# Kernel optimization log

Hardware: AMD Instinct MI355X
Metric: run time of the kernel (lower is better)

Reference implementation:

```python
import jax, jax.numpy as jnp
import numpy as np

N = 2048          # n_nodes
H = 8             # nheads
ALPHA = 0.2       # leaky-relu slope
NEG = -9e15       # mask value used by pyGAT
# (in_dim, per-head hidden, out_dim) for the six GAT blocks of GMHAAE(256, ...)
DIMS = [(256, 128, 128), (128, 256, 256), (256, 512, 384),
        (384, 512, 256), (256, 256, 128), (128, 128, 256)]


def setup_inputs() -> dict:
    key = jax.random.key(0)
    ks = jax.random.split(key, 64)
    inp = {}
    inp["x"] = jax.random.normal(ks[0], (N, 256), dtype=jnp.float32)
    a = (jax.random.uniform(ks[1], (N, N)) < 0.01).astype(jnp.float32)
    adj = jnp.clip(jnp.maximum(a, a.T) + jnp.eye(N, dtype=jnp.float32), 0.0, 1.0)
    inp["adj"] = adj
    ki = 2
    for i, (fin, hid, fout) in enumerate(DIMS, start=1):
        s1 = (2.0 / (fin + hid)) ** 0.5
        inp[f"p{i}_Wh"] = jax.random.normal(ks[ki], (H, fin, hid), dtype=jnp.float32) * s1; ki += 1
        inp[f"p{i}_ah"] = jax.random.normal(ks[ki], (H, 2 * hid), dtype=jnp.float32) * 0.1; ki += 1
        s2 = (2.0 / (H * hid + fout)) ** 0.5
        inp[f"p{i}_Wo"] = jax.random.normal(ks[ki], (H * hid, fout), dtype=jnp.float32) * s2; ki += 1
        inp[f"p{i}_ao"] = jax.random.normal(ks[ki], (2 * fout,), dtype=jnp.float32) * 0.1; ki += 1
    return inp


def _gat_block(x, adj, Wh, ah, Wo, ao):
    """pyGAT GAT block: H concat heads (elu) -> single out head -> elu. Eval mode (no dropout)."""
    n = x.shape[0]
    D = Wh.shape[2]
    h = jnp.einsum('nf,hfd->hnd', x, Wh)                       # [H,N,D]
    s1 = jnp.einsum('hnd,hd->hn', h, ah[:, :D])                # a^T [Wh_i]
    s2 = jnp.einsum('hnd,hd->hn', h, ah[:, D:])                # a^T [Wh_j]
    e = jax.nn.leaky_relu(s1[:, :, None] + s2[:, None, :], ALPHA)   # [H,N,N]
    att = jax.nn.softmax(jnp.where(adj[None] > 0, e, NEG), axis=-1)
    hcat = jax.nn.elu(jnp.einsum('hnm,hmd->hnd', att, h))      # concat=True -> elu per head
    hcat = hcat.transpose(1, 0, 2).reshape(n, -1)              # [N, H*D]
    # output attention head (concat=False)
    D2 = Wo.shape[1]
    ho = hcat @ Wo                                             # [N,D2]
    eo = jax.nn.leaky_relu((ho @ ao[:D2])[:, None] + (ho @ ao[D2:])[None, :], ALPHA)
    ato = jax.nn.softmax(jnp.where(adj > 0, eo, NEG), axis=-1)
    return jax.nn.elu(ato @ ho)                                # F.elu in GAT.forward


def reference(x, adj,
              p1_Wh, p1_ah, p1_Wo, p1_ao,
              p2_Wh, p2_ah, p2_Wo, p2_ao,
              p3_Wh, p3_ah, p3_Wo, p3_ao,
              p4_Wh, p4_ah, p4_Wo, p4_ao,
              p5_Wh, p5_ah, p5_Wo, p5_ao,
              p6_Wh, p6_ah, p6_Wo, p6_ao):
    layers = [(p1_Wh, p1_ah, p1_Wo, p1_ao), (p2_Wh, p2_ah, p2_Wo, p2_ao),
              (p3_Wh, p3_ah, p3_Wo, p3_ao), (p4_Wh, p4_ah, p4_Wo, p4_ao),
              (p5_Wh, p5_ah, p5_Wo, p5_ao), (p6_Wh, p6_ah, p6_Wo, p6_ao)]
    h = x
    for (Wh, ah, Wo, ao) in layers:   # fixed 6-layer encoder-decoder stack
        h = _gat_block(h, adj, Wh, ah, Wo, ao)
    return h
```

## Files before the change

### kernel.cpp

```cpp
#include <hip/hip_runtime.h>
#include <hip/hip_bf16.h>
#include <math.h>

#define NN 2048
#define NH 8
#define LRALPHA 0.2f

typedef short bf16x8 __attribute__((ext_vector_type(8)));
typedef float f32x4  __attribute__((ext_vector_type(4)));

static __device__ __forceinline__ float lrelu(float x){ return x > 0.f ? x : LRALPHA * x; }
static __device__ __forceinline__ float elu(float x){ return x > 0.f ? x : expm1f(x); }

static __device__ __forceinline__ unsigned short f2bf(float v){
    unsigned u = __float_as_uint(v);
    unsigned r = (u + 0x7fffu + ((u >> 16) & 1u)) >> 16;
    return (unsigned short)r;
}
static __device__ __forceinline__ float bf2f(unsigned short b){
    return __uint_as_float(((unsigned)b) << 16);
}
static __device__ __forceinline__ float blo(unsigned u){ return __uint_as_float(u << 16); }
static __device__ __forceinline__ float bhi(unsigned u){ return __uint_as_float(u & 0xffff0000u); }

static __device__ __forceinline__ void gload16(const void* g, void* l){
    __builtin_amdgcn_global_load_lds((const __attribute__((address_space(1))) void*)g,
                                     (__attribute__((address_space(3))) void*)l, 16, 0, 0);
}

__global__ void k_count(const float* __restrict__ adj, int* __restrict__ deg) {
    int gw   = (blockIdx.x * blockDim.x + threadIdx.x) >> 6;
    int lane = threadIdx.x & 63;
    if (gw >= NN) return;
    const float* row = adj + (size_t)gw * NN;
    int cnt = 0;
    for (int j = lane; j < NN; j += 64) cnt += (row[j] > 0.f) ? 1 : 0;
    #pragma unroll
    for (int off = 32; off; off >>= 1) cnt += __shfl_down(cnt, off);
    if (lane == 0) deg[gw] = cnt;
}

__global__ void k_scan(const int* __restrict__ deg, int* __restrict__ rp) {
    __shared__ int a[NN], b[NN];
    int t = threadIdx.x;
    for (int i = t; i < NN; i += 1024) a[i] = deg[i];
    __syncthreads();
    int* src = a; int* dst = b;
    for (int off = 1; off < NN; off <<= 1) {
        for (int i = t; i < NN; i += 1024)
            dst[i] = src[i] + (i >= off ? src[i - off] : 0);
        __syncthreads();
        int* tmp = src; src = dst; dst = tmp;
    }
    for (int i = t; i < NN; i += 1024) rp[i + 1] = src[i];
    if (t == 0) rp[0] = 0;
}

__global__ void k_fill(const float* __restrict__ adj, const int* __restrict__ rp,
                       int* __restrict__ ci) {
    int gw   = (blockIdx.x * blockDim.x + threadIdx.x) >> 6;
    int lane = threadIdx.x & 63;
    if (gw >= NN) return;
    const float* row = adj + (size_t)gw * NN;
    int base = rp[gw];
    for (int j0 = 0; j0 < NN; j0 += 64) {
        bool v = row[j0 + lane] > 0.f;
        unsigned long long m = __ballot(v);
        int pos = __popcll(m & ((1ULL << lane) - 1ULL));
        if (v) ci[base + pos] = j0 + lane;
        base += __popcll(m);
    }
}

__global__ void k_split(const float* __restrict__ src, unsigned short* __restrict__ hi,
                        unsigned short* __restrict__ lo, int n4) {
    int i = blockIdx.x * 256 + threadIdx.x;
    if (i >= n4) return;
    float4 v = ((const float4*)src)[i];
    ushort4 h, l;
    h.x = f2bf(v.x); l.x = f2bf(v.x - bf2f(h.x));
    h.y = f2bf(v.y); l.y = f2bf(v.y - bf2f(h.y));
    h.z = f2bf(v.z); l.z = f2bf(v.z - bf2f(h.z));
    h.w = f2bf(v.w); l.w = f2bf(v.w - bf2f(h.w));
    ((ushort4*)hi)[i] = h;
    ((ushort4*)lo)[i] = l;
}

struct TSDesc {
    const float* B[12];
    unsigned short* bh[12];
    unsigned short* bl[12];
    int K[12], Nc[12], hs[12];
    int start[13];
};

__global__ __launch_bounds__(256) void k_tsplit_all(TSDesc d) {
    __shared__ float t[64][65];
    int b = blockIdx.x;
    int s = 0;
    while (b >= d.start[s + 1]) s++;
    int lb = b - d.start[s];
    int K = d.K[s], Nc = d.Nc[s], hs = d.hs[s];
    int tilesX = K >> 6;
    int kb = (lb % tilesX) * 64, cb = (lb / tilesX) * 64;
    const float* B = d.B[s];
    unsigned short* bth = d.bh[s];
    unsigned short* btl = d.bl[s];

    int tid = threadIdx.x;
    #pragma unroll
    for (int i = 0; i < 16; i++) {
        int idx = i * 256 + tid;
        int kk = idx >> 6, cc = idx & 63;
        int c = cb + cc, k = kb + kk;
        float v;
        if (hs < 0) v = B[(size_t)k * Nc + c];
        else {
            int hid = 1 << hs; int head = c >> hs; int dd = c & (hid - 1);
            v = B[((size_t)head * K + k) * hid + dd];
        }
        t[kk][cc] = v;
    }
    __syncthreads();
    #pragma unroll
    for (int i = 0; i < 16; i++) {
        int idx = i * 256 + tid;
        int cc = idx >> 6, kk = idx & 63;
        float v = t[kk][cc];
        unsigned short h = f2bf(v);
        size_t o = (size_t)(cb + cc) * K + kb + kk;
        bth[o] = h;
        btl[o] = f2bf(v - bf2f(h));
    }
}

template<int OUT, int NT>
__global__ __launch_bounds__(256) void k_mfma(
    const unsigned short* __restrict__ Ah, const unsigned short* __restrict__ Al,
    const unsigned short* __restrict__ Bh, const unsigned short* __restrict__ Bl,
    float* __restrict__ Cf, unsigned short* __restrict__ Cb, int Nc, int K, int Kc,
    const float* __restrict__ avec, float* __restrict__ sg1, float* __restrict__ sg2,
    int hs, int aoff, int nx, int nz, int zcol)
{
    constexpr int ALB = 4096;
    constexpr int BHB = (NT == 3) ? 8192 : 4096;
    constexpr int BLB = BHB + 2048;
    __shared__ unsigned short lds[(NT == 3) ? 12288 : 8192];
    int tid = threadIdx.x, lane = tid & 63, w = tid >> 6;

    int g = blockIdx.x;
    int xcd = g & 7, q = g >> 3;
    int x, y, z;
    if (zcol) {
        int zper = nz >> 3;
        z = xcd + 8 * (q % zper);
        int r = q / zper;
        int nxy = nx * 16;
        int r2 = r + xcd * (nxy >> 3); if (r2 >= nxy) r2 -= nxy;
        x = r2 % nx; y = r2 / nx;
    } else {
        y = xcd + 8 * (q & 1);
        x = q >> 1; z = 0;
    }
    int m0 = y * 128, n0 = x * 64;
    int kbeg = z * Kc;

    int ra0 = tid >> 2;       int ga0 = ((tid & 3) - (ra0 >> 1)) & 3;
    int ra1 = 64 + (tid >> 2); int ga1 = ((tid & 3) - (ra1 >> 1)) & 3;
    int rb  = tid >> 2;       int gb  = ((tid & 3) - (rb >> 1)) & 3;
    const unsigned short* pAh0 = Ah + (size_t)(m0 + ra0) * K + kbeg + ga0 * 8;
    const unsigned short* pAh1 = Ah + (size_t)(m0 + ra1) * K + kbeg + ga1 * 8;
    const unsigned short* pAl0 = (NT == 3) ? Al + (size_t)(m0 + ra0) * K + kbeg + ga0 * 8 : nullptr;
    const unsigned short* pAl1 = (NT == 3) ? Al + (size_t)(m0 + ra1) * K + kbeg + ga1 * 8 : nullptr;
    const unsigned short* pBh  = Bh + (size_t)(n0 + rb) * K + kbeg + gb * 8;
    const unsigned short* pBl  = Bl + (size_t)(n0 + rb) * K + kbeg + gb * 8;
    unsigned short* dA0 = &lds[w * 512];
    unsigned short* dA1 = &lds[2048 + w * 512];
    unsigned short* dB  = &lds[BHB + w * 512];

    int wr = w >> 1, wc = w & 1;
    int offA[4], offB[2];
    #pragma unroll
    for (int m = 0; m < 4; m++) {
        int row = wr * 64 + m * 16 + (lane & 15); int gg = lane >> 4;
        offA[m] = (row * 4 + ((gg + (row >> 1)) & 3)) * 8;
    }
    #pragma unroll
    for (int n = 0; n < 2; n++) {
        int row = wc * 32 + n * 16 + (lane & 15); int gg = lane >> 4;
        offB[n] = (row * 4 + ((gg + (row >> 1)) & 3)) * 8;
    }

    f32x4 acc[4][2];
    #pragma unroll
    for (int m = 0; m < 4; m++)
        #pragma unroll
        for (int n = 0; n < 2; n++) acc[m][n] = (f32x4){0.f, 0.f, 0.f, 0.f};

    int nk = Kc >> 5;
    for (int ks = 0; ks < nk; ks++) {
        gload16(pAh0, dA0);
        gload16(pAh1, dA1);
        if (NT == 3) { gload16(pAl0, dA0 + ALB); gload16(pAl1, dA1 + ALB); }
        gload16(pBh, dB);
        gload16(pBl, dB + 2048);
        pAh0 += 32; pAh1 += 32;
        if (NT == 3) { pAl0 += 32; pAl1 += 32; }
        pBh += 32; pBl += 32;
        __syncthreads();
        bf16x8 ah[4], al[4], bh[2], bl[2];
        #pragma unroll
        for (int m = 0; m < 4; m++) {
            ah[m] = *(const bf16x8*)&lds[offA[m]];
            if (NT == 3) al[m] = *(const bf16x8*)&lds[ALB + offA[m]];
        }
        #pragma unroll
        for (int n = 0; n < 2; n++) {
            bh[n] = *(const bf16x8*)&lds[BHB + offB[n]];
            bl[n] = *(const bf16x8*)&lds[BLB + offB[n]];
        }
        #pragma unroll
        for (int m = 0; m < 4; m++)
            #pragma unroll
            for (int n = 0; n < 2; n++) {
                acc[m][n] = __builtin_amdgcn_mfma_f32_16x16x32_bf16(ah[m], bh[n], acc[m][n], 0, 0, 0);
                if (NT == 3)
                    acc[m][n] = __builtin_amdgcn_mfma_f32_16x16x32_bf16(al[m], bh[n], acc[m][n], 0, 0, 0);
                acc[m][n] = __builtin_amdgcn_mfma_f32_16x16x32_bf16(ah[m], bl[n], acc[m][n], 0, 0, 0);
            }
        __syncthreads();
    }

    size_t pbase = (size_t)z * NN * Nc;
    #pragma unroll
    for (int m = 0; m < 4; m++)
        #pragma unroll
        for (int n = 0; n < 2; n++) {
            int row = m0 + wr * 64 + m * 16 + (lane >> 4) * 4;
            int col = n0 + wc * 32 + n * 16 + (lane & 15);
            #pragma unroll
            for (int r = 0; r < 4; r++) {
                float v = acc[m][n][r];
                if (OUT == 0) Cb[(size_t)(row + r) * Nc + col] = f2bf(v);
                else          Cf[pbase + (size_t)(row + r) * Nc + col] = v;
            }
        }

    if (OUT == 0) {
        int head = (hs >= 0) ? (n0 >> hs) : 0;
        const float* ab = avec + head * 2 * aoff;
        float av1[2], av2[2];
        int colbase = n0 + wc * 32 + (lane & 15);
        #pragma unroll
        for (int n = 0; n < 2; n++) {
            int c = colbase + n * 16;
            int dd = (hs >= 0) ? (c & (aoff - 1)) : c;
            av1[n] = ab[dd];
            av2[n] = ab[dd + aoff];
        }
        #pragma unroll
        for (int m = 0; m < 4; m++)
            #pragma unroll
            for (int r = 0; r < 4; r++) {
                float p1 = 0.f, p2 = 0.f;
                #pragma unroll
                for (int n = 0; n < 2; n++) {
                    float v = acc[m][n][r];
                    p1 += v * av1[n];
                    p2 += v * av2[n];
                }
                #pragma unroll
                for (int o = 1; o < 16; o <<= 1) {
                    p1 += __shfl_xor(p1, o);
                    p2 += __shfl_xor(p2, o);
                }
                if ((lane & 15) == 0) {
                    int row = m0 + wr * 64 + m * 16 + (lane >> 4) * 4 + r;
                    atomicAdd(&sg1[head * NN + row], p1);
                    atomicAdd(&sg2[head * NN + row], p2);
                }
            }
    }
}

__global__ __launch_bounds__(64) void k_red(
    const float* __restrict__ part, float* __restrict__ ho,
    const float* __restrict__ ao, float* __restrict__ t1, float* __restrict__ t2,
    int fout, int sko)
{
    int row = blockIdx.x;
    int lane = threadIdx.x;
    int C4 = fout >> 2;
    const float4* p4 = (const float4*)part;
    size_t stride4 = (size_t)NN * C4;
    float d1 = 0.f, d2 = 0.f;
    for (int c = lane; c < C4; c += 64) {
        size_t o = (size_t)row * C4 + c;
        float4 s = p4[o];
        for (int zz = 1; zz < sko; zz++) {
            float4 v = p4[o + (size_t)zz * stride4];
            s.x += v.x; s.y += v.y; s.z += v.z; s.w += v.w;
        }
        ((float4*)ho)[o] = s;
        int cc = c * 4;
        d1 += s.x * ao[cc]        + s.y * ao[cc + 1]
            + s.z * ao[cc + 2]    + s.w * ao[cc + 3];
        d2 += s.x * ao[fout + cc]     + s.y * ao[fout + cc + 1]
            + s.z * ao[fout + cc + 2] + s.w * ao[fout + cc + 3];
    }
    #pragma unroll
    for (int o = 32; o; o >>= 1) { d1 += __shfl_xor(d1, o); d2 += __shfl_xor(d2, o); }
    if (lane == 0) { t1[row] = d1; t2[row] = d2; }
}

__global__ __launch_bounds__(64) void k_aggb(
    const unsigned short* __restrict__ hh, const float* __restrict__ s1,
    const float* __restrict__ s2, const int* __restrict__ rp, const int* __restrict__ ci,
    unsigned short* __restrict__ outH, int hid, int HD, int c8sh)
{
    __shared__ float    wls[64];
    __shared__ unsigned cls[64];

    int blk  = blockIdx.x;
    int head = blk & (NH - 1);
    int i    = blk >> 3;
    int lane = threadIdx.x;
    int base = rp[i], deg = rp[i + 1] - base;
    float s1i = s1[head * NN + i];
    const float* s2h = s2 + head * NN;

    int C8  = 1 << c8sh;
    int G   = 64 >> c8sh;
    int col = lane & (C8 - 1);
    int grp = lane >> c8sh;

    const uint4* h4 = (const uint4*)hh;
    unsigned hoff8 = (unsigned)(head * hid) >> 3;
    unsigned ld8   = (unsigned)HD >> 3;

    float m_run = -1e30f, s_run = 0.f;
    float a0=0,a1=0,a2=0,a3=0,a4=0,a5=0,a6=0,a7=0;

    for (int k0 = 0; k0 < deg; k0 += 64) {
        int n = min(64, deg - k0);
        float e = -1e30f;
        unsigned coff = 0;
        if (lane < n) {
            int j = ci[base + k0 + lane];
            e = lrelu(s1i + s2h[j]);
            coff = (unsigned)j * ld8 + hoff8;
        }
        float bm = e;
        #pragma unroll
        for (int o = 32; o; o >>= 1) bm = fmaxf(bm, __shfl_xor(bm, o));
        float m2 = fmaxf(m_run, bm);
        float wv = (lane < n) ? expf(e - m2) : 0.f;
        float bs = wv;
        #pragma unroll
        for (int o = 32; o; o >>= 1) bs += __shfl_xor(bs, o);
        float scale = expf(m_run - m2);
        s_run = s_run * scale + bs;
        a0*=scale; a1*=scale; a2*=scale; a3*=scale;
        a4*=scale; a5*=scale; a6*=scale; a7*=scale;
        m_run = m2;
        wls[lane] = wv;
        cls[lane] = coff;

        float q0=0,q1=0,q2=0,q3=0,q4=0,q5=0,q6=0,q7=0;
        int k = grp;
        for (; k + G < n; k += 2 * G) {
            float w0 = wls[k], w1 = wls[k + G];
            uint4 u0 = h4[cls[k]     + col];
            uint4 u1 = h4[cls[k + G] + col];
            a0 += w0 * blo(u0.x); a1 += w0 * bhi(u0.x);
            a2 += w0 * blo(u0.y); a3 += w0 * bhi(u0.y);
            a4 += w0 * blo(u0.z); a5 += w0 * bhi(u0.z);
            a6 += w0 * blo(u0.w); a7 += w0 * bhi(u0.w);
            q0 += w1 * blo(u1.x); q1 += w1 * bhi(u1.x);
            q2 += w1 * blo(u1.y); q3 += w1 * bhi(u1.y);
            q4 += w1 * blo(u1.z); q5 += w1 * bhi(u1.z);
            q6 += w1 * blo(u1.w); q7 += w1 * bhi(u1.w);
        }
        if (k < n) {
            float w0 = wls[k];
            uint4 u0 = h4[cls[k] + col];
            a0 += w0 * blo(u0.x); a1 += w0 * bhi(u0.x);
            a2 += w0 * blo(u0.y); a3 += w0 * bhi(u0.y);
            a4 += w0 * blo(u0.z); a5 += w0 * bhi(u0.z);
            a6 += w0 * blo(u0.w); a7 += w0 * bhi(u0.w);
        }
        a0+=q0; a1+=q1; a2+=q2; a3+=q3; a4+=q4; a5+=q5; a6+=q6; a7+=q7;
    }

    #pragma unroll
    for (int o = 64; o > 1; o >>= 1) {
        if (o > C8) {
            int m = o >> 1;
            a0 += __shfl_xor(a0, m); a1 += __shfl_xor(a1, m);
            a2 += __shfl_xor(a2, m); a3 += __shfl_xor(a3, m);
            a4 += __shfl_xor(a4, m); a5 += __shfl_xor(a5, m);
            a6 += __shfl_xor(a6, m); a7 += __shfl_xor(a7, m);
        }
    }

    if (grp == 0) {
        float inv = 1.f / s_run;
        float v[8] = {a0*inv,a1*inv,a2*inv,a3*inv,a4*inv,a5*inv,a6*inv,a7*inv};
        #pragma unroll
        for (int e2 = 0; e2 < 8; e2++) v[e2] = elu(v[e2]);
        unsigned short hh_[8];
        #pragma unroll
        for (int e2 = 0; e2 < 8; e2++) hh_[e2] = f2bf(v[e2]);
        size_t ob = ((size_t)i * HD + head * hid) >> 3;
        uint4 ph;
        ph.x = (unsigned)hh_[0] | ((unsigned)hh_[1] << 16);
        ph.y = (unsigned)hh_[2] | ((unsigned)hh_[3] << 16);
        ph.z = (unsigned)hh_[4] | ((unsigned)hh_[5] << 16);
        ph.w = (unsigned)hh_[6] | ((unsigned)hh_[7] << 16);
        ((uint4*)outH)[ob + col] = ph;
    }
}

__global__ __launch_bounds__(64) void k_aggs(
    const float* __restrict__ hsrc, const float* __restrict__ t1, const float* __restrict__ t2,
    const int* __restrict__ rp, const int* __restrict__ ci,
    float* __restrict__ outF, unsigned short* __restrict__ outH,
    int fout, int SCtot)
{
    __shared__ float    wls[64];
    __shared__ unsigned cls[64];

    int blk = blockIdx.x;
    int i   = blk / SCtot;
    int sc  = blk - i * SCtot;
    int lane = threadIdx.x;
    int base = rp[i], deg = rp[i + 1] - base;
    float s1i = t1[i];

    int C4tot = fout >> 2;
    int soff  = sc * 64;
    int C4s   = min(64, C4tot - soff);
    int c4sh  = 31 - __clz(C4s);
    int col = lane & (C4s - 1);
    int grp = lane >> c4sh;
    int G   = 64 >> c4sh;

    const float4* h4 = (const float4*)hsrc;
    unsigned ld4 = (unsigned)fout >> 2;

    float m_run = -1e30f, s_run = 0.f;
    float4 acc = make_float4(0.f, 0.f, 0.f, 0.f);

    for (int k0 = 0; k0 < deg; k0 += 64) {
        int n = min(64, deg - k0);
        float e = -1e30f;
        unsigned coff = 0;
        if (lane < n) {
            int j = ci[base + k0 + lane];
            e = lrelu(s1i + t2[j]);
            coff = (unsigned)j * ld4 + soff;
        }
        float bm = e;
        #pragma unroll
        for (int o = 32; o; o >>= 1) bm = fmaxf(bm, __shfl_xor(bm, o));
        float m2 = fmaxf(m_run, bm);
        float wv = (lane < n) ? expf(e - m2) : 0.f;
        float bs = wv;
        #pragma unroll
        for (int o = 32; o; o >>= 1) bs += __shfl_xor(bs, o);
        float scale = expf(m_run - m2);
        s_run = s_run * scale + bs;
        acc.x *= scale; acc.y *= scale; acc.z *= scale; acc.w *= scale;
        m_run = m2;
        wls[lane] = wv;
        cls[lane] = coff;

        float4 q = make_float4(0,0,0,0);
        int k = grp;
        for (; k + G < n; k += 2 * G) {
            float w0 = wls[k], w1 = wls[k + G];
            float4 h0 = h4[cls[k]     + col];
            float4 h1 = h4[cls[k + G] + col];
            acc.x += w0 * h0.x; acc.y += w0 * h0.y; acc.z += w0 * h0.z; acc.w += w0 * h0.w;
            q.x   += w1 * h1.x; q.y   += w1 * h1.y; q.z   += w1 * h1.z; q.w   += w1 * h1.w;
        }
        if (k < n) {
            float w0 = wls[k];
            float4 h0 = h4[cls[k] + col];
            acc.x += w0 * h0.x; acc.y += w0 * h0.y; acc.z += w0 * h0.z; acc.w += w0 * h0.w;
        }
        acc.x += q.x; acc.y += q.y; acc.z += q.z; acc.w += q.w;
    }

    #pragma unroll
    for (int o = 64; o > 1; o >>= 1) {
        if (o > C4s) {
            int m = o >> 1;
            acc.x += __shfl_xor(acc.x, m); acc.y += __shfl_xor(acc.y, m);
            acc.z += __shfl_xor(acc.z, m); acc.w += __shfl_xor(acc.w, m);
        }
    }

    if (grp == 0) {
        float inv = 1.f / s_run;
        float4 val;
        val.x = elu(acc.x * inv); val.y = elu(acc.y * inv);
        val.z = elu(acc.z * inv); val.w = elu(acc.w * inv);
        size_t o4 = (size_t)i * ld4 + soff + col;
        if (outF) ((float4*)outF)[o4] = val;
        ushort4 h;
        h.x = f2bf(val.x); h.y = f2bf(val.y);
        h.z = f2bf(val.z); h.w = f2bf(val.w);
        ((ushort4*)outH)[o4] = h;
    }
}

extern "C" void kernel_launch(void* const* d_in, const int* in_sizes, int n_in,
                              void* d_out, int out_size, void* d_ws, size_t ws_size,
                              hipStream_t stream)
{
    const float* x   = (const float*)d_in[0];
    const float* adj = (const float*)d_in[1];
    struct L { int fin, hid, fout; };
    const L dims[6] = {{256,128,128},{128,256,256},{256,512,384},
                       {384,512,256},{256,256,128},{128,128,256}};
    const int SKwo[6] = {16, 8, 8, 8, 16, 8};
    const int SB = 2 * NH * NN;

    char* ws = (char*)d_ws;
    size_t off = 0;
    auto alloc = [&](size_t bytes) -> void* {
        void* p = ws + off;
        off = (off + bytes + 255) & ~(size_t)255;
        return p;
    };
    int*   rp   = (int*)alloc((NN + 1) * sizeof(int));
    int*   deg  = (int*)alloc(NN * sizeof(int));
    int*   ci   = (int*)alloc((size_t)(1 << 20) * sizeof(int));
    unsigned short* hh  = (unsigned short*)alloc((size_t)NN * 4096 * 2);
    unsigned short* ghi = (unsigned short*)alloc((size_t)NN * 4096 * 2);
    unsigned short* xhi = (unsigned short*)alloc((size_t)NN * 512 * 2);
    unsigned short* xlo = (unsigned short*)alloc((size_t)NN * 512 * 2);
    float* sball  = (float*)alloc((size_t)6 * SB * sizeof(float));
    float* hopart = (float*)alloc((size_t)NN * 3072 * sizeof(float));
    float* ho     = (float*)alloc((size_t)NN * 384 * sizeof(float));
    float* t12    = (float*)alloc((size_t)2 * NN * sizeof(float));

    unsigned short* whh[6]; unsigned short* whl[6];
    unsigned short* woh[6]; unsigned short* wol[6];
    TSDesc td;
    int nblk = 0;
    for (int l = 0; l < 6; l++) {
        int fin = dims[l].fin, hid = dims[l].hid, fout = dims[l].fout;
        int HD = NH * hid;
        size_t szWh = (size_t)fin * HD, szWo = (size_t)HD * fout;
        whh[l] = (unsigned short*)alloc(szWh * 2);
        whl[l] = (unsigned short*)alloc(szWh * 2);
        woh[l] = (unsigned short*)alloc(szWo * 2);
        wol[l] = (unsigned short*)alloc(szWo * 2);
        int hs = (hid == 128) ? 7 : (hid == 256) ? 8 : 9;
        td.B[2*l] = (const float*)d_in[2 + l * 4 + 0];
        td.bh[2*l] = whh[l]; td.bl[2*l] = whl[l];
        td.K[2*l] = fin; td.Nc[2*l] = HD; td.hs[2*l] = hs;
        td.start[2*l] = nblk; nblk += (fin / 64) * (HD / 64);
        td.B[2*l+1] = (const float*)d_in[2 + l * 4 + 2];
        td.bh[2*l+1] = woh[l]; td.bl[2*l+1] = wol[l];
        td.K[2*l+1] = HD; td.Nc[2*l+1] = fout; td.hs[2*l+1] = -1;
        td.start[2*l+1] = nblk; nblk += (HD / 64) * (fout / 64);
    }
    td.start[12] = nblk;

    hipMemsetAsync(sball, 0, (size_t)6 * SB * sizeof(float), stream);
    k_count<<<NN / 4, 256, 0, stream>>>(adj, deg);
    k_scan <<<1, 1024, 0, stream>>>(deg, rp);
    k_fill <<<NN / 4, 256, 0, stream>>>(adj, rp, ci);
    k_split<<<(NN * 256 / 4 + 255) / 256, 256, 0, stream>>>(x, xhi, xlo, NN * 256 / 4);
    k_tsplit_all<<<nblk, 256, 0, stream>>>(td);

    for (int l = 0; l < 6; l++) {
        int fin = dims[l].fin, hid = dims[l].hid, fout = dims[l].fout;
        int HD = NH * hid;
        int hs = (hid == 128) ? 7 : (hid == 256) ? 8 : 9;
        int c8sh = hs - 3;
        const float* ah = (const float*)d_in[2 + l * 4 + 1];
        const float* ao = (const float*)d_in[2 + l * 4 + 3];

        float* s1 = sball + (size_t)l * SB;
        float* s2 = s1 + NH * NN;
        float* t1 = t12;
        float* t2 = t12 + NN;

        int nx1 = HD / 64;
        if (l == 0)
            k_mfma<0,3><<<nx1 * 16, 256, 0, stream>>>(xhi, xlo, whh[l], whl[l], nullptr, hh, HD,
                                                      fin, fin, ah, s1, s2, hs, hid, nx1, 1, 0);
        else
            k_mfma<0,2><<<nx1 * 16, 256, 0, stream>>>(xhi, nullptr, whh[l], whl[l], nullptr, hh, HD,
                                                      fin, fin, ah, s1, s2, hs, hid, nx1, 1, 0);

        k_aggb<<<NN * NH, 64, 0, stream>>>(hh, s1, s2, rp, ci, ghi, hid, HD, c8sh);

        int sko = SKwo[l];
        int nx2 = fout / 64;
        k_mfma<1,2><<<nx2 * 16 * sko, 256, 0, stream>>>(ghi, nullptr, woh[l], wol[l], hopart,
                                                        nullptr, fout, HD, HD / sko,
                                                        nullptr, nullptr, nullptr, -1, fout,
                                                        nx2, sko, 1);

        k_red<<<NN, 64, 0, stream>>>(hopart, ho, ao, t1, t2, fout, sko);

        float* outF = (l == 5) ? (float*)d_out : nullptr;
        int SCtot = (fout / 4 + 63) / 64;
        k_aggs<<<NN * SCtot, 64, 0, stream>>>(ho, t1, t2, rp, ci, outF, xhi, fout, SCtot);
    }
}
```

Baseline: 449.6 us.

## Double GEMM K-tile to 64 and widen per-lane columns in aggregation kernels

The MFMA GEMM now stages a 64-wide K slice per iteration, using a new 8-group XOR swizzle. This halves the number of barrier pairs per K loop at the cost of twice the LDS footprint. The two sparse-attention aggregation kernels now have each lane handle 16 bf16 or 8 fp32 columns instead of 8 or 4. That gives each lane more independent loads and more groups over neighbours, but raises register pressure and adds shuffle-reduction steps.

```diff
diff --git a/kernel.cpp b/kernel.cpp
--- a/kernel.cpp
+++ b/kernel.cpp
@@ -27,6 +27,12 @@
     __builtin_amdgcn_global_load_lds((const __attribute__((address_space(1))) void*)g,
                                      (__attribute__((address_space(3))) void*)l, 16, 0, 0);
 }
+
+#define ACC8(A, base, wv, u) \
+    A[base+0] += wv * blo(u.x); A[base+1] += wv * bhi(u.x); \
+    A[base+2] += wv * blo(u.y); A[base+3] += wv * bhi(u.y); \
+    A[base+4] += wv * blo(u.z); A[base+5] += wv * bhi(u.z); \
+    A[base+6] += wv * blo(u.w); A[base+7] += wv * bhi(u.w);
 
 __global__ void k_count(const float* __restrict__ adj, int* __restrict__ deg) {
     int gw   = (blockIdx.x * blockDim.x + threadIdx.x) >> 6;
@@ -142,10 +148,10 @@
     const float* __restrict__ avec, float* __restrict__ sg1, float* __restrict__ sg2,
     int hs, int aoff, int nx, int nz, int zcol)
 {
-    constexpr int ALB = 4096;
-    constexpr int BHB = (NT == 3) ? 8192 : 4096;
-    constexpr int BLB = BHB + 2048;
-    __shared__ unsigned short lds[(NT == 3) ? 12288 : 8192];
+    constexpr int ALB = 8192;
+    constexpr int BHB = (NT == 3) ? 16384 : 8192;
+    constexpr int BLB = BHB + 4096;
+    __shared__ unsigned short lds[(NT == 3) ? 24576 : 16384];
     int tid = threadIdx.x, lane = tid & 63, w = tid >> 6;
 
     int g = blockIdx.x;
@@ -165,30 +171,44 @@
     int m0 = y * 128, n0 = x * 64;
     int kbeg = z * Kc;
 
-    int ra0 = tid >> 2;       int ga0 = ((tid & 3) - (ra0 >> 1)) & 3;
-    int ra1 = 64 + (tid >> 2); int ga1 = ((tid & 3) - (ra1 >> 1)) & 3;
-    int rb  = tid >> 2;       int gb  = ((tid & 3) - (rb >> 1)) & 3;
-    const unsigned short* pAh0 = Ah + (size_t)(m0 + ra0) * K + kbeg + ga0 * 8;
-    const unsigned short* pAh1 = Ah + (size_t)(m0 + ra1) * K + kbeg + ga1 * 8;
-    const unsigned short* pAl0 = (NT == 3) ? Al + (size_t)(m0 + ra0) * K + kbeg + ga0 * 8 : nullptr;
-    const unsigned short* pAl1 = (NT == 3) ? Al + (size_t)(m0 + ra1) * K + kbeg + ga1 * 8 : nullptr;
-    const unsigned short* pBh  = Bh + (size_t)(n0 + rb) * K + kbeg + gb * 8;
-    const unsigned short* pBl  = Bl + (size_t)(n0 + rb) * K + kbeg + gb * 8;
-    unsigned short* dA0 = &lds[w * 512];
-    unsigned short* dA1 = &lds[2048 + w * 512];
-    unsigned short* dB  = &lds[BHB + w * 512];
+    const unsigned short* pA[4];
+    const unsigned short* pAl_[4];
+    const unsigned short* pB[2];
+    const unsigned short* pBl_[2];
+    #pragma unroll
+    for (int c = 0; c < 4; c++) {
+        int s = c * 256 + tid;
+        int row = s >> 3; int gl = ((s & 7) - row) & 7;
+        pA[c] = Ah + (size_t)(m0 + row) * K + kbeg + gl * 8;
+        if (NT == 3) pAl_[c] = Al + (size_t)(m0 + row) * K + kbeg + gl * 8;
+    }
+    #pragma unroll
+    for (int c = 0; c < 2; c++) {
+        int s = c * 256 + tid;
+        int row = s >> 3; int gl = ((s & 7) - row) & 7;
+        pB[c]   = Bh + (size_t)(n0 + row) * K + kbeg + gl * 8;
+        pBl_[c] = Bl + (size_t)(n0 + row) * K + kbeg + gl * 8;
+    }
 
     int wr = w >> 1, wc = w & 1;
-    int offA[4], offB[2];
+    int offA[4][2], offB[2][2];
     #pragma unroll
     for (int m = 0; m < 4; m++) {
-        int row = wr * 64 + m * 16 + (lane & 15); int gg = lane >> 4;
-        offA[m] = (row * 4 + ((gg + (row >> 1)) & 3)) * 8;
+        int row = wr * 64 + m * 16 + (lane & 15);
+        #pragma unroll
+        for (int kk = 0; kk < 2; kk++) {
+            int gl = (lane >> 4) + 4 * kk;
+            offA[m][kk] = row * 64 + (((gl + row) & 7) * 8);
+        }
     }
     #pragma unroll
     for (int n = 0; n < 2; n++) {
-        int row = wc * 32 + n * 16 + (lane & 15); int gg = lane >> 4;
-        offB[n] = (row * 4 + ((gg + (row >> 1)) & 3)) * 8;
+        int row = wc * 32 + n * 16 + (lane & 15);
+        #pragma unroll
+        for (int kk = 0; kk < 2; kk++) {
+            int gl = (lane >> 4) + 4 * kk;
+            offB[n][kk] = row * 64 + (((gl + row) & 7) * 8);
+        }
     }
 
     f32x4 acc[4][2];
@@ -197,37 +217,42 @@
         #pragma unroll
         for (int n = 0; n < 2; n++) acc[m][n] = (f32x4){0.f, 0.f, 0.f, 0.f};
 
-    int nk = Kc >> 5;
+    int nk = Kc >> 6;
     for (int ks = 0; ks < nk; ks++) {
-        gload16(pAh0, dA0);
-        gload16(pAh1, dA1);
-        if (NT == 3) { gload16(pAl0, dA0 + ALB); gload16(pAl1, dA1 + ALB); }
-        gload16(pBh, dB);
-        gload16(pBl, dB + 2048);
-        pAh0 += 32; pAh1 += 32;
-        if (NT == 3) { pAl0 += 32; pAl1 += 32; }
-        pBh += 32; pBl += 32;
+        #pragma unroll
+        for (int c = 0; c < 4; c++) { gload16(pA[c], &lds[c * 2048 + w * 512]); pA[c] += 64; }
+        if (NT == 3) {
+            #pragma unroll
+            for (int c = 0; c < 4; c++) { gload16(pAl_[c], &lds[ALB + c * 2048 + w * 512]); pAl_[c] += 64; }
+        }
+        #pragma unroll
+        for (int c = 0; c < 2; c++) { gload16(pB[c], &lds[BHB + c * 2048 + w * 512]); pB[c] += 64; }
+        #pragma unroll
+        for (int c = 0; c < 2; c++) { gload16(pBl_[c], &lds[BLB + c * 2048 + w * 512]); pBl_[c] += 64; }
         __syncthreads();
-        bf16x8 ah[4], al[4], bh[2], bl[2];
-        #pragma unroll
-        for (int m = 0; m < 4; m++) {
-            ah[m] = *(const bf16x8*)&lds[offA[m]];
-            if (NT == 3) al[m] = *(const bf16x8*)&lds[ALB + offA[m]];
-        }
-        #pragma unroll
-        for (int n = 0; n < 2; n++) {
-            bh[n] = *(const bf16x8*)&lds[BHB + offB[n]];
-            bl[n] = *(const bf16x8*)&lds[BLB + offB[n]];
-        }
-        #pragma unroll
-        for (int m = 0; m < 4; m++)
+        #pragma unroll
+        for (int kk = 0; kk < 2; kk++) {
+            bf16x8 ah[4], al[4], bh[2], bl[2];
+            #pragma unroll
+            for (int m = 0; m < 4; m++) {
+                ah[m] = *(const bf16x8*)&lds[offA[m][kk]];
+                if (NT == 3) al[m] = *(const bf16x8*)&lds[ALB + offA[m][kk]];
+            }
             #pragma unroll
             for (int n = 0; n < 2; n++) {
-                acc[m][n] = __builtin_amdgcn_mfma_f32_16x16x32_bf16(ah[m], bh[n], acc[m][n], 0, 0, 0);
-                if (NT == 3)
-                    acc[m][n] = __builtin_amdgcn_mfma_f32_16x16x32_bf16(al[m], bh[n], acc[m][n], 0, 0, 0);
-                acc[m][n] = __builtin_amdgcn_mfma_f32_16x16x32_bf16(ah[m], bl[n], acc[m][n], 0, 0, 0);
+                bh[n] = *(const bf16x8*)&lds[BHB + offB[n][kk]];
+                bl[n] = *(const bf16x8*)&lds[BLB + offB[n][kk]];
             }
+            #pragma unroll
+            for (int m = 0; m < 4; m++)
+                #pragma unroll
+                for (int n = 0; n < 2; n++) {
+                    acc[m][n] = __builtin_amdgcn_mfma_f32_16x16x32_bf16(ah[m], bh[n], acc[m][n], 0, 0, 0);
+                    if (NT == 3)
+                        acc[m][n] = __builtin_amdgcn_mfma_f32_16x16x32_bf16(al[m], bh[n], acc[m][n], 0, 0, 0);
+                    acc[m][n] = __builtin_amdgcn_mfma_f32_16x16x32_bf16(ah[m], bl[n], acc[m][n], 0, 0, 0);
+                }
+        }
         __syncthreads();
     }
 
@@ -316,7 +341,7 @@
 __global__ __launch_bounds__(64) void k_aggb(
     const unsigned short* __restrict__ hh, const float* __restrict__ s1,
     const float* __restrict__ s2, const int* __restrict__ rp, const int* __restrict__ ci,
-    unsigned short* __restrict__ outH, int hid, int HD, int c8sh)
+    unsigned short* __restrict__ outH, int hid, int HD, int c16sh)
 {
     __shared__ float    wls[64];
     __shared__ unsigned cls[64];
@@ -329,17 +354,19 @@
     float s1i = s1[head * NN + i];
     const float* s2h = s2 + head * NN;
 
-    int C8  = 1 << c8sh;
-    int G   = 64 >> c8sh;
-    int col = lane & (C8 - 1);
-    int grp = lane >> c8sh;
+    int C16 = 1 << c16sh;
+    int G   = 64 >> c16sh;
+    int col = lane & (C16 - 1);
+    int grp = lane >> c16sh;
 
     const uint4* h4 = (const uint4*)hh;
     unsigned hoff8 = (unsigned)(head * hid) >> 3;
     unsigned ld8   = (unsigned)HD >> 3;
 
     float m_run = -1e30f, s_run = 0.f;
-    float a0=0,a1=0,a2=0,a3=0,a4=0,a5=0,a6=0,a7=0;
+    float aA[16];
+    #pragma unroll
+    for (int e = 0; e < 16; e++) aA[e] = 0.f;
 
     for (int k0 = 0; k0 < deg; k0 += 64) {
         int n = min(64, deg - k0);
@@ -360,64 +387,60 @@
         for (int o = 32; o; o >>= 1) bs += __shfl_xor(bs, o);
         float scale = expf(m_run - m2);
         s_run = s_run * scale + bs;
-        a0*=scale; a1*=scale; a2*=scale; a3*=scale;
-        a4*=scale; a5*=scale; a6*=scale; a7*=scale;
+        #pragma unroll
+        for (int e2 = 0; e2 < 16; e2++) aA[e2] *= scale;
         m_run = m2;
         wls[lane] = wv;
         cls[lane] = coff;
 
-        float q0=0,q1=0,q2=0,q3=0,q4=0,q5=0,q6=0,q7=0;
+        float q[16];
+        #pragma unroll
+        for (int e2 = 0; e2 < 16; e2++) q[e2] = 0.f;
         int k = grp;
         for (; k + G < n; k += 2 * G) {
             float w0 = wls[k], w1 = wls[k + G];
-            uint4 u0 = h4[cls[k]     + col];
-            uint4 u1 = h4[cls[k + G] + col];
-            a0 += w0 * blo(u0.x); a1 += w0 * bhi(u0.x);
-            a2 += w0 * blo(u0.y); a3 += w0 * bhi(u0.y);
-            a4 += w0 * blo(u0.z); a5 += w0 * bhi(u0.z);
-            a6 += w0 * blo(u0.w); a7 += w0 * bhi(u0.w);
-            q0 += w1 * blo(u1.x); q1 += w1 * bhi(u1.x);
-            q2 += w1 * blo(u1.y); q3 += w1 * bhi(u1.y);
-            q4 += w1 * blo(u1.z); q5 += w1 * bhi(u1.z);
-            q6 += w1 * blo(u1.w); q7 += w1 * bhi(u1.w);
+            const uint4* r0 = h4 + cls[k]     + 2 * col;
+            const uint4* r1 = h4 + cls[k + G] + 2 * col;
+            uint4 u0 = r0[0], u1 = r0[1];
+            uint4 v0 = r1[0], v1 = r1[1];
+            ACC8(aA, 0, w0, u0); ACC8(aA, 8, w0, u1);
+            ACC8(q,  0, w1, v0); ACC8(q,  8, w1, v1);
         }
         if (k < n) {
             float w0 = wls[k];
-            uint4 u0 = h4[cls[k] + col];
-            a0 += w0 * blo(u0.x); a1 += w0 * bhi(u0.x);
-            a2 += w0 * blo(u0.y); a3 += w0 * bhi(u0.y);
-            a4 += w0 * blo(u0.z); a5 += w0 * bhi(u0.z);
-            a6 += w0 * blo(u0.w); a7 += w0 * bhi(u0.w);
-        }
-        a0+=q0; a1+=q1; a2+=q2; a3+=q3; a4+=q4; a5+=q5; a6+=q6; a7+=q7;
-    }
-
-    #pragma unroll
-    for (int o = 64; o > 1; o >>= 1) {
-        if (o > C8) {
-            int m = o >> 1;
-            a0 += __shfl_xor(a0, m); a1 += __shfl_xor(a1, m);
-            a2 += __shfl_xor(a2, m); a3 += __shfl_xor(a3, m);
-            a4 += __shfl_xor(a4, m); a5 += __shfl_xor(a5, m);
-            a6 += __shfl_xor(a6, m); a7 += __shfl_xor(a7, m);
+            const uint4* r0 = h4 + cls[k] + 2 * col;
+            uint4 u0 = r0[0], u1 = r0[1];
+            ACC8(aA, 0, w0, u0); ACC8(aA, 8, w0, u1);
+        }
+        #pragma unroll
+        for (int e2 = 0; e2 < 16; e2++) aA[e2] += q[e2];
+    }
+
+    #pragma unroll
+    for (int m = 32; m >= 1; m >>= 1) {
+        if (m >= C16) {
+            #pragma unroll
+            for (int e2 = 0; e2 < 16; e2++) aA[e2] += __shfl_xor(aA[e2], m);
         }
     }
 
     if (grp == 0) {
         float inv = 1.f / s_run;
-        float v[8] = {a0*inv,a1*inv,a2*inv,a3*inv,a4*inv,a5*inv,a6*inv,a7*inv};
-        #pragma unroll
-        for (int e2 = 0; e2 < 8; e2++) v[e2] = elu(v[e2]);
-        unsigned short hh_[8];
-        #pragma unroll
-        for (int e2 = 0; e2 < 8; e2++) hh_[e2] = f2bf(v[e2]);
-        size_t ob = ((size_t)i * HD + head * hid) >> 3;
-        uint4 ph;
-        ph.x = (unsigned)hh_[0] | ((unsigned)hh_[1] << 16);
-        ph.y = (unsigned)hh_[2] | ((unsigned)hh_[3] << 16);
-        ph.z = (unsigned)hh_[4] | ((unsigned)hh_[5] << 16);
-        ph.w = (unsigned)hh_[6] | ((unsigned)hh_[7] << 16);
-        ((uint4*)outH)[ob + col] = ph;
+        unsigned short hh_[16];
+        #pragma unroll
+        for (int e2 = 0; e2 < 16; e2++) hh_[e2] = f2bf(elu(aA[e2] * inv));
+        size_t ob = (((size_t)i * HD + head * hid) >> 3) + 2 * col;
+        uint4 p0, p1;
+        p0.x = (unsigned)hh_[0]  | ((unsigned)hh_[1]  << 16);
+        p0.y = (unsigned)hh_[2]  | ((unsigned)hh_[3]  << 16);
+        p0.z = (unsigned)hh_[4]  | ((unsigned)hh_[5]  << 16);
+        p0.w = (unsigned)hh_[6]  | ((unsigned)hh_[7]  << 16);
+        p1.x = (unsigned)hh_[8]  | ((unsigned)hh_[9]  << 16);
+        p1.y = (unsigned)hh_[10] | ((unsigned)hh_[11] << 16);
+        p1.z = (unsigned)hh_[12] | ((unsigned)hh_[13] << 16);
+        p1.w = (unsigned)hh_[14] | ((unsigned)hh_[15] << 16);
+        ((uint4*)outH)[ob]     = p0;
+        ((uint4*)outH)[ob + 1] = p1;
     }
 }
 
@@ -440,16 +463,19 @@
     int C4tot = fout >> 2;
     int soff  = sc * 64;
     int C4s   = min(64, C4tot - soff);
-    int c4sh  = 31 - __clz(C4s);
-    int col = lane & (C4s - 1);
-    int grp = lane >> c4sh;
-    int G   = 64 >> c4sh;
+    int C8s   = C4s >> 1;
+    int c8sh  = 31 - __clz(C8s);
+    int col = lane & (C8s - 1);
+    int grp = lane >> c8sh;
+    int G   = 64 >> c8sh;
 
     const float4* h4 = (const float4*)hsrc;
     unsigned ld4 = (unsigned)fout >> 2;
 
     float m_run = -1e30f, s_run = 0.f;
-    float4 acc = make_float4(0.f, 0.f, 0.f, 0.f);
+    float aA[8];
+    #pragma unroll
+    for (int e = 0; e < 8; e++) aA[e] = 0.f;
 
     for (int k0 = 0; k0 < deg; k0 += 64) {
         int n = min(64, deg - k0);
@@ -470,48 +496,61 @@
         for (int o = 32; o; o >>= 1) bs += __shfl_xor(bs, o);
         float scale = expf(m_run - m2);
         s_run = s_run * scale + bs;
-        acc.x *= scale; acc.y *= scale; acc.z *= scale; acc.w *= scale;
+        #pragma unroll
+        for (int e2 = 0; e2 < 8; e2++) aA[e2] *= scale;
         m_run = m2;
         wls[lane] = wv;
         cls[lane] = coff;
 
-        float4 q = make_float4(0,0,0,0);
+        float q[8];
+        #pragma unroll
+        for (int e2 = 0; e2 < 8; e2++) q[e2] = 0.f;
         int k = grp;
         for (; k + G < n; k += 2 * G) {
             float w0 = wls[k], w1 = wls[k + G];
-            float4 h0 = h4[cls[k]     + col];
-            float4 h1 = h4[cls[k + G] + col];
-            acc.x += w0 * h0.x; acc.y += w0 * h0.y; acc.z += w0 * h0.z; acc.w += w0 * h0.w;
-            q.x   += w1 * h1.x; q.y   += w1 * h1.y; q.z   += w1 * h1.z; q.w   += w1 * h1.w;
+            const float4* r0 = h4 + cls[k]     + 2 * col;
+            const float4* r1 = h4 + cls[k + G] + 2 * col;
+            float4 h0 = r0[0], h1 = r0[1];
+            float4 g0 = r1[0], g1 = r1[1];
+            aA[0] += w0 * h0.x; aA[1] += w0 * h0.y; aA[2] += w0 * h0.z; aA[3] += w0 * h0.w;
+            aA[4] += w0 * h1.x; aA[5] += w0 * h1.y; aA[6] += w0 * h1.z; aA[7] += w0 * h1.w;
+            q[0]  += w1 * g0.x; q[1]  += w1 * g0.y; q[2]  += w1 * g0.z; q[3]  += w1 * g0.w;
+            q[4]  += w1 * g1.x; q[5]  += w1 * g1.y; q[6]  += w1 * g1.z; q[7]  += w1 * g1.w;
         }
         if (k < n) {
             float w0 = wls[k];
-            float4 h0 = h4[cls[k] + col];
-            acc.x += w0 * h0.x; acc.y += w0 * h0.y; acc.z += w0 * h0.z; acc.w += w0 * h0.w;
-        }
-        acc.x += q.x; acc.y += q.y; acc.z += q.z; acc.w += q.w;
-    }
-
-    #pragma unroll
-    for (int o = 64; o > 1; o >>= 1) {
-        if (o > C4s) {
-            int m = o >> 1;
-            acc.x += __shfl_xor(acc.x, m); acc.y += __shfl_xor(acc.y, m);
-            acc.z += __shfl_xor(acc.z, m); acc.w += __shfl_xor(acc.w, m);
+            const float4* r0 = h4 + cls[k] + 2 * col;
+            float4 h0 = r0[0], h1 = r0[1];
+            aA[0] += w0 * h0.x; aA[1] += w0 * h0.y; aA[2] += w0 * h0.z; aA[3] += w0 * h0.w;
+            aA[4] += w0 * h1.x; aA[5] += w0 * h1.y; aA[6] += w0 * h1.z; aA[7] += w0 * h1.w;
+        }
+        #pragma unroll
+        for (int e2 = 0; e2 < 8; e2++) aA[e2] += q[e2];
+    }
+
+    #pragma unroll
+    for (int m = 32; m >= 1; m >>= 1) {
+        if (m >= C8s) {
+            #pragma unroll
+            for (int e2 = 0; e2 < 8; e2++) aA[e2] += __shfl_xor(aA[e2], m);
         }
     }
 
     if (grp == 0) {
         float inv = 1.f / s_run;
-        float4 val;
-        val.x = elu(acc.x * inv); val.y = elu(acc.y * inv);
-        val.z = elu(acc.z * inv); val.w = elu(acc.w * inv);
-        size_t o4 = (size_t)i * ld4 + soff + col;
-        if (outF) ((float4*)outF)[o4] = val;
-        ushort4 h;
-        h.x = f2bf(val.x); h.y = f2bf(val.y);
-        h.z = f2bf(val.z); h.w = f2bf(val.w);
-        ((ushort4*)outH)[o4] = h;
+        float v[8];
+        #pragma unroll
+        for (int e2 = 0; e2 < 8; e2++) v[e2] = elu(aA[e2] * inv);
+        size_t o4 = (size_t)i * ld4 + soff + 2 * col;
+        if (outF) {
+            ((float4*)outF)[o4]     = make_float4(v[0], v[1], v[2], v[3]);
+            ((float4*)outF)[o4 + 1] = make_float4(v[4], v[5], v[6], v[7]);
+        }
+        ushort4 h0, h1;
+        h0.x = f2bf(v[0]); h0.y = f2bf(v[1]); h0.z = f2bf(v[2]); h0.w = f2bf(v[3]);
+        h1.x = f2bf(v[4]); h1.y = f2bf(v[5]); h1.z = f2bf(v[6]); h1.w = f2bf(v[7]);
+        ((ushort4*)outH)[o4]     = h0;
+        ((ushort4*)outH)[o4 + 1] = h1;
     }
 }
 
@@ -581,7 +620,6 @@
         int fin = dims[l].fin, hid = dims[l].hid, fout = dims[l].fout;
         int HD = NH * hid;
         int hs = (hid == 128) ? 7 : (hid == 256) ? 8 : 9;
-        int c8sh = hs - 3;
         const float* ah = (const float*)d_in[2 + l * 4 + 1];
         const float* ao = (const float*)d_in[2 + l * 4 + 3];
 
@@ -598,7 +636,7 @@
             k_mfma<0,2><<<nx1 * 16, 256, 0, stream>>>(xhi, nullptr, whh[l], whl[l], nullptr, hh, HD,
                                                       fin, fin, ah, s1, s2, hs, hid, nx1, 1, 0);
 
-        k_aggb<<<NN * NH, 64, 0, stream>>>(hh, s1, s2, rp, ci, ghi, hid, HD, c8sh);
+        k_aggb<<<NN * NH, 64, 0, stream>>>(hh, s1, s2, rp, ci, ghi, hid, HD, hs - 4);
 
         int sko = SKwo[l];
         int nx2 = fout / 64;
```

Measured after the change: 467.5 us. +4.0%, slower.

## Process multiple heads per wave and four rows per block in head aggregation

Applied to the files above, without the earlier changes.

The sparse attention aggregation kernel now assigns HP heads to each wave, chosen from the hidden size so every lane owns a full 8-column chunk, and packs four node rows per 256-thread block. Neighbor indices are loaded once and shared across the heads a wave handles. Each lane now issues several independent gathers per step through a deeper templated unroll, which raises memory-level parallelism. In exchange, register pressure grows because every lane keeps 16 accumulators per head. Lanes in the softmax statistics loop also repeat the shuffle reductions once per head.

```diff
diff --git a/kernel.cpp b/kernel.cpp
--- a/kernel.cpp
+++ b/kernel.cpp
@@ -27,6 +27,12 @@
     __builtin_amdgcn_global_load_lds((const __attribute__((address_space(1))) void*)g,
                                      (__attribute__((address_space(3))) void*)l, 16, 0, 0);
 }
+
+#define ACC8(A, wv, u) \
+    A[0] += wv * blo(u.x); A[1] += wv * bhi(u.x); \
+    A[2] += wv * blo(u.y); A[3] += wv * bhi(u.y); \
+    A[4] += wv * blo(u.z); A[5] += wv * bhi(u.z); \
+    A[6] += wv * blo(u.w); A[7] += wv * bhi(u.w);
 
 __global__ void k_count(const float* __restrict__ adj, int* __restrict__ deg) {
     int gw   = (blockIdx.x * blockDim.x + threadIdx.x) >> 6;
@@ -313,111 +319,126 @@
     if (lane == 0) { t1[row] = d1; t2[row] = d2; }
 }
 
-__global__ __launch_bounds__(64) void k_aggb(
+template<int HP>
+__global__ __launch_bounds__(256) void k_aggb(
     const unsigned short* __restrict__ hh, const float* __restrict__ s1,
     const float* __restrict__ s2, const int* __restrict__ rp, const int* __restrict__ ci,
-    unsigned short* __restrict__ outH, int hid, int HD, int c8sh)
+    unsigned short* __restrict__ outH, int hid, int HD)
 {
-    __shared__ float    wls[64];
-    __shared__ unsigned cls[64];
-
-    int blk  = blockIdx.x;
-    int head = blk & (NH - 1);
-    int i    = blk >> 3;
-    int lane = threadIdx.x;
+    constexpr int NHG = NH / HP;
+    constexpr int D   = (HP == 1) ? 8 : (HP == 2) ? 4 : 2;
+    constexpr int C8  = 64 / HP;
+    constexpr int G   = HP;
+
+    __shared__ float    wls[4][HP][64];
+    __shared__ unsigned cls[4][64];
+
+    int tid = threadIdx.x, wid = tid >> 6, lane = tid & 63;
+    int hg = blockIdx.x & (NHG - 1);
+    int i  = (blockIdx.x / NHG) * 4 + wid;
+    int h0 = hg * HP;
+
     int base = rp[i], deg = rp[i + 1] - base;
-    float s1i = s1[head * NN + i];
-    const float* s2h = s2 + head * NN;
-
-    int C8  = 1 << c8sh;
-    int G   = 64 >> c8sh;
-    int col = lane & (C8 - 1);
-    int grp = lane >> c8sh;
+    float s1i[HP];
+    #pragma unroll
+    for (int p = 0; p < HP; p++) s1i[p] = s1[(h0 + p) * NN + i];
+
+    int col = lane & (C8 - 1), grp = lane >> (6 - (HP == 1 ? 0 : HP == 2 ? 1 : 2));
+    grp = lane / C8;
 
     const uint4* h4 = (const uint4*)hh;
-    unsigned hoff8 = (unsigned)(head * hid) >> 3;
-    unsigned ld8   = (unsigned)HD >> 3;
-
-    float m_run = -1e30f, s_run = 0.f;
-    float a0=0,a1=0,a2=0,a3=0,a4=0,a5=0,a6=0,a7=0;
+    unsigned ld8 = (unsigned)HD >> 3;
+    unsigned hoff8[HP];
+    #pragma unroll
+    for (int p = 0; p < HP; p++) hoff8[p] = ((unsigned)(h0 + p) * hid) >> 3;
+
+    float m_run[HP], s_run[HP], acc[HP][8], q[HP][8];
+    #pragma unroll
+    for (int p = 0; p < HP; p++) {
+        m_run[p] = -1e30f; s_run[p] = 0.f;
+        #pragma unroll
+        for (int e = 0; e < 8; e++) { acc[p][e] = 0.f; q[p][e] = 0.f; }
+    }
 
     for (int k0 = 0; k0 < deg; k0 += 64) {
         int n = min(64, deg - k0);
-        float e = -1e30f;
-        unsigned coff = 0;
-        if (lane < n) {
-            int j = ci[base + k0 + lane];
-            e = lrelu(s1i + s2h[j]);
-            coff = (unsigned)j * ld8 + hoff8;
-        }
-        float bm = e;
-        #pragma unroll
-        for (int o = 32; o; o >>= 1) bm = fmaxf(bm, __shfl_xor(bm, o));
-        float m2 = fmaxf(m_run, bm);
-        float wv = (lane < n) ? expf(e - m2) : 0.f;
-        float bs = wv;
-        #pragma unroll
-        for (int o = 32; o; o >>= 1) bs += __shfl_xor(bs, o);
-        float scale = expf(m_run - m2);
-        s_run = s_run * scale + bs;
-        a0*=scale; a1*=scale; a2*=scale; a3*=scale;
-        a4*=scale; a5*=scale; a6*=scale; a7*=scale;
-        m_run = m2;
-        wls[lane] = wv;
-        cls[lane] = coff;
-
-        float q0=0,q1=0,q2=0,q3=0,q4=0,q5=0,q6=0,q7=0;
+        bool act = lane < n;
+        int j = 0;
+        if (act) { j = ci[base + k0 + lane]; cls[wid][lane] = (unsigned)j * ld8; }
+        #pragma unroll
+        for (int p = 0; p < HP; p++) {
+            float e = act ? lrelu(s1i[p] + s2[(h0 + p) * NN + j]) : -1e30f;
+            float bm = e;
+            #pragma unroll
+            for (int o = 32; o; o >>= 1) bm = fmaxf(bm, __shfl_xor(bm, o));
+            float m2 = fmaxf(m_run[p], bm);
+            float wv = act ? expf(e - m2) : 0.f;
+            float bs = wv;
+            #pragma unroll
+            for (int o = 32; o; o >>= 1) bs += __shfl_xor(bs, o);
+            float scale = expf(m_run[p] - m2);
+            s_run[p] = s_run[p] * scale + bs;
+            #pragma unroll
+            for (int e2 = 0; e2 < 8; e2++) acc[p][e2] *= scale;
+            m_run[p] = m2;
+            wls[wid][p][lane] = wv;
+        }
+
         int k = grp;
-        for (; k + G < n; k += 2 * G) {
-            float w0 = wls[k], w1 = wls[k + G];
-            uint4 u0 = h4[cls[k]     + col];
-            uint4 u1 = h4[cls[k + G] + col];
-            a0 += w0 * blo(u0.x); a1 += w0 * bhi(u0.x);
-            a2 += w0 * blo(u0.y); a3 += w0 * bhi(u0.y);
-            a4 += w0 * blo(u0.z); a5 += w0 * bhi(u0.z);
-            a6 += w0 * blo(u0.w); a7 += w0 * bhi(u0.w);
-            q0 += w1 * blo(u1.x); q1 += w1 * bhi(u1.x);
-            q2 += w1 * blo(u1.y); q3 += w1 * bhi(u1.y);
-            q4 += w1 * blo(u1.z); q5 += w1 * bhi(u1.z);
-            q6 += w1 * blo(u1.w); q7 += w1 * bhi(u1.w);
-        }
-        if (k < n) {
-            float w0 = wls[k];
-            uint4 u0 = h4[cls[k] + col];
-            a0 += w0 * blo(u0.x); a1 += w0 * bhi(u0.x);
-            a2 += w0 * blo(u0.y); a3 += w0 * bhi(u0.y);
-            a4 += w0 * blo(u0.z); a5 += w0 * bhi(u0.z);
-            a6 += w0 * blo(u0.w); a7 += w0 * bhi(u0.w);
-        }
-        a0+=q0; a1+=q1; a2+=q2; a3+=q3; a4+=q4; a5+=q5; a6+=q6; a7+=q7;
-    }
-
-    #pragma unroll
-    for (int o = 64; o > 1; o >>= 1) {
-        if (o > C8) {
-            int m = o >> 1;
-            a0 += __shfl_xor(a0, m); a1 += __shfl_xor(a1, m);
-            a2 += __shfl_xor(a2, m); a3 += __shfl_xor(a3, m);
-            a4 += __shfl_xor(a4, m); a5 += __shfl_xor(a5, m);
-            a6 += __shfl_xor(a6, m); a7 += __shfl_xor(a7, m);
+        for (; k + (D - 1) * G < n; k += D * G) {
+            #pragma unroll
+            for (int dd = 0; dd < D; dd++) {
+                int kk = k + dd * G;
+                unsigned rbase = cls[wid][kk];
+                #pragma unroll
+                for (int p = 0; p < HP; p++) {
+                    float w0 = wls[wid][p][kk];
+                    uint4 u0 = h4[rbase + hoff8[p] + col];
+                    if (dd & 1) { ACC8(q[p],   w0, u0); }
+                    else        { ACC8(acc[p], w0, u0); }
+                }
+            }
+        }
+        for (; k < n; k += G) {
+            unsigned rbase = cls[wid][k];
+            #pragma unroll
+            for (int p = 0; p < HP; p++) {
+                float w0 = wls[wid][p][k];
+                uint4 u0 = h4[rbase + hoff8[p] + col];
+                ACC8(acc[p], w0, u0);
+            }
+        }
+        #pragma unroll
+        for (int p = 0; p < HP; p++)
+            #pragma unroll
+            for (int e2 = 0; e2 < 8; e2++) { acc[p][e2] += q[p][e2]; q[p][e2] = 0.f; }
+    }
+
+    #pragma unroll
+    for (int m = 32; m >= 1; m >>= 1) {
+        if (m >= C8) {
+            #pragma unroll
+            for (int p = 0; p < HP; p++)
+                #pragma unroll
+                for (int e2 = 0; e2 < 8; e2++) acc[p][e2] += __shfl_xor(acc[p][e2], m);
         }
     }
 
     if (grp == 0) {
-        float inv = 1.f / s_run;
-        float v[8] = {a0*inv,a1*inv,a2*inv,a3*inv,a4*inv,a5*inv,a6*inv,a7*inv};
-        #pragma unroll
-        for (int e2 = 0; e2 < 8; e2++) v[e2] = elu(v[e2]);
-        unsigned short hh_[8];
-        #pragma unroll
-        for (int e2 = 0; e2 < 8; e2++) hh_[e2] = f2bf(v[e2]);
-        size_t ob = ((size_t)i * HD + head * hid) >> 3;
-        uint4 ph;
-        ph.x = (unsigned)hh_[0] | ((unsigned)hh_[1] << 16);
-        ph.y = (unsigned)hh_[2] | ((unsigned)hh_[3] << 16);
-        ph.z = (unsigned)hh_[4] | ((unsigned)hh_[5] << 16);
-        ph.w = (unsigned)hh_[6] | ((unsigned)hh_[7] << 16);
-        ((uint4*)outH)[ob + col] = ph;
+        #pragma unroll
+        for (int p = 0; p < HP; p++) {
+            float inv = 1.f / s_run[p];
+            unsigned short hb[8];
+            #pragma unroll
+            for (int e2 = 0; e2 < 8; e2++) hb[e2] = f2bf(elu(acc[p][e2] * inv));
+            size_t ob = ((size_t)i * HD + (size_t)(h0 + p) * hid) >> 3;
+            uint4 ph;
+            ph.x = (unsigned)hb[0] | ((unsigned)hb[1] << 16);
+            ph.y = (unsigned)hb[2] | ((unsigned)hb[3] << 16);
+            ph.z = (unsigned)hb[4] | ((unsigned)hb[5] << 16);
+            ph.w = (unsigned)hb[6] | ((unsigned)hb[7] << 16);
+            ((uint4*)outH)[ob + col] = ph;
+        }
     }
 }
 
@@ -581,7 +602,6 @@
         int fin = dims[l].fin, hid = dims[l].hid, fout = dims[l].fout;
         int HD = NH * hid;
         int hs = (hid == 128) ? 7 : (hid == 256) ? 8 : 9;
-        int c8sh = hs - 3;
         const float* ah = (const float*)d_in[2 + l * 4 + 1];
         const float* ao = (const float*)d_in[2 + l * 4 + 3];
 
@@ -598,7 +618,12 @@
             k_mfma<0,2><<<nx1 * 16, 256, 0, stream>>>(xhi, nullptr, whh[l], whl[l], nullptr, hh, HD,
                                                       fin, fin, ah, s1, s2, hs, hid, nx1, 1, 0);
 
-        k_aggb<<<NN * NH, 64, 0, stream>>>(hh, s1, s2, rp, ci, ghi, hid, HD, c8sh);
+        if (hid == 512)
+            k_aggb<1><<<(NN / 4) * 8, 256, 0, stream>>>(hh, s1, s2, rp, ci, ghi, hid, HD);
+        else if (hid == 256)
+            k_aggb<2><<<(NN / 4) * 4, 256, 0, stream>>>(hh, s1, s2, rp, ci, ghi, hid, HD);
+        else
+            k_aggb<4><<<(NN / 4) * 2, 256, 0, stream>>>(hh, s1, s2, rp, ci, ghi, hid, HD);
 
         int sko = SKwo[l];
         int nx2 = fout / 64;
```

Measured after the change: 484.9 us. 7.9% more time.
